# Kernel tuning notes

Measured on AMD Instinct MI355X. Metric: run time of the kernel, lower is better.

## Reference

```python
import jax, jax.numpy as jnp
import numpy as np

N_NODES = 50000
N_EDGES = 312500
WIDTH = 256
LN_EPS = 1e-5


def setup_inputs() -> dict:
    key = jax.random.key(0)
    k1, k2, k3, k4 = jax.random.split(key, 4)
    x = jax.random.normal(k1, (N_NODES, WIDTH), dtype=jnp.float32)
    edge_index = jax.random.randint(k2, (2, N_EDGES), 0, N_NODES, dtype=jnp.int64)
    # GCNConv linear weight (out, in) and bias, LayerNorm affine params
    W = jax.random.normal(k3, (WIDTH, WIDTH), dtype=jnp.float32) / np.sqrt(WIDTH)
    b = jax.random.normal(k4, (WIDTH,), dtype=jnp.float32) * 0.01
    gamma = jnp.ones((WIDTH,), dtype=jnp.float32)
    beta = jnp.zeros((WIDTH,), dtype=jnp.float32)
    return {"x": x, "edge_index": edge_index, "W": W, "b": b, "gamma": gamma, "beta": beta}


def gcn_conv(x, edge_index, W, b):
    """PyG GCNConv: add self-loops, symmetric normalization, scatter-add aggregate."""
    n = x.shape[0]
    loops = jnp.arange(n, dtype=edge_index.dtype)
    src = jnp.concatenate([edge_index[0], loops])  # message source
    dst = jnp.concatenate([edge_index[1], loops])  # message destination
    # degree computed on destination nodes (including self-loops)
    deg = jax.ops.segment_sum(jnp.ones_like(dst, dtype=x.dtype), dst, num_segments=n)
    dinv = jnp.where(deg > 0, jax.lax.rsqrt(deg), 0.0)
    norm = dinv[src] * dinv[dst]  # [E+N]
    h = x @ W.T  # [N, width]
    msgs = norm[:, None] * h[src]  # [E+N, width]
    out = jax.ops.segment_sum(msgs, dst, num_segments=n)
    return out + b


def layer_norm(x, gamma, beta):
    mu = jnp.mean(x, axis=-1, keepdims=True)
    var = jnp.mean(jnp.square(x - mu), axis=-1, keepdims=True)
    return (x - mu) * jax.lax.rsqrt(var + LN_EPS) * gamma + beta


def reference(x, edge_index, W, b, gamma, beta):
    h = gcn_conv(x, edge_index, W, b)
    h = layer_norm(h, gamma, beta)
    h = jax.nn.relu(h)
    # dropout is identity in eval mode
    return h
```

## Files before the change

kernel.cpp:

```cpp
#include <hip/hip_runtime.h>
#include <hip/hip_bf16.h>

#define N_NODES 50000
#define N_EDGES 312500
#define WIDTH   256
#define LN_EPS  1e-5f
#define NB_SCAN 196

typedef __attribute__((ext_vector_type(8))) short bf16x8;
typedef __attribute__((ext_vector_type(4))) float f32x4;

__device__ __forceinline__ float bf_lo(unsigned u) { return __uint_as_float(u << 16); }
__device__ __forceinline__ float bf_hi(unsigned u) { return __uint_as_float(u & 0xffff0000u); }

__global__ void count_dst(const int* __restrict__ dst, int* __restrict__ counts, int e) {
    int i = blockIdx.x * blockDim.x + threadIdx.x;
    if (i < e) atomicAdd(&counts[dst[i]], 1);
}

__global__ __launch_bounds__(256) void scan_pass_a(const int* __restrict__ counts,
                                                   int* __restrict__ block_sums, int n) {
    int t = threadIdx.x;
    int i = blockIdx.x * 256 + t;
    int v = (i < n) ? counts[i] : 0;
    #pragma unroll
    for (int off = 32; off > 0; off >>= 1) v += __shfl_down(v, off, 64);
    __shared__ int ws[4];
    if ((t & 63) == 0) ws[t >> 6] = v;
    __syncthreads();
    if (t == 0) block_sums[blockIdx.x] = ws[0] + ws[1] + ws[2] + ws[3];
}

__global__ __launch_bounds__(256) void scan_pass_b(int* __restrict__ block_sums, int nb) {
    int t = threadIdx.x;
    int lane = t & 63, w = t >> 6;
    int v = (t < nb) ? block_sums[t] : 0;
    int inc = v;
    #pragma unroll
    for (int off = 1; off < 64; off <<= 1) {
        int u = __shfl_up(inc, off, 64);
        if (lane >= off) inc += u;
    }
    __shared__ int wsum[4];
    if (lane == 63) wsum[w] = inc;
    __syncthreads();
    int woff = 0;
    for (int k = 0; k < 4; k++) if (k < w) woff += wsum[k];
    if (t < nb) block_sums[t] = inc - v + woff;
}

__global__ __launch_bounds__(256) void scan_pass_c(int* __restrict__ counts,
                                                   const int* __restrict__ block_sums,
                                                   int* __restrict__ offsets,
                                                   float* __restrict__ dinv, int n) {
    int t = threadIdx.x;
    int i = blockIdx.x * 256 + t;
    int lane = t & 63, w = t >> 6;
    int v = (i < n) ? counts[i] : 0;
    int inc = v;
    #pragma unroll
    for (int off = 1; off < 64; off <<= 1) {
        int u = __shfl_up(inc, off, 64);
        if (lane >= off) inc += u;
    }
    __shared__ int wsum[4];
    if (lane == 63) wsum[w] = inc;
    __syncthreads();
    int woff = 0;
    for (int k = 0; k < 4; k++) if (k < w) woff += wsum[k];
    int excl = block_sums[blockIdx.x] + inc - v + woff;
    if (i < n) {
        offsets[i] = excl;
        counts[i]  = excl;
        dinv[i]    = rsqrtf((float)(v + 1));
    }
    if (i == n - 1) offsets[n] = N_EDGES;
}

__global__ void fill_csr(const int* __restrict__ src, const int* __restrict__ dst,
                         const float* __restrict__ dinv,
                         int* __restrict__ cursor, int2* __restrict__ csr2, int e) {
    int i = blockIdx.x * blockDim.x + threadIdx.x;
    if (i < e) {
        int s = src[i];
        int pos = atomicAdd(&cursor[dst[i]], 1);
        csr2[pos] = make_int2(s, __float_as_int(dinv[s]));
    }
}

__global__ __launch_bounds__(256) void gemm_mfma(const float* __restrict__ x,
                                                 const float* __restrict__ W,
                                                 __hip_bfloat16* __restrict__ h) {
    __shared__ short As[128][72];
    __shared__ short Bs[128][72];
    const int t    = threadIdx.x;
    const int lane = t & 63;
    const int wv   = t >> 6;
    const int wm   = wv & 1;
    const int wn   = wv >> 1;
    const int lrow = lane & 15;
    const int quad = lane >> 4;
    const int mrow0 = blockIdx.x * 128;
    const int ncol0 = blockIdx.y * 128;

    f32x4 acc[4][4];
    #pragma unroll
    for (int i = 0; i < 4; i++)
        #pragma unroll
        for (int j = 0; j < 4; j++)
            #pragma unroll
            for (int r = 0; r < 4; r++) acc[i][j][r] = 0.0f;

    const int sr = t >> 3;
    const int sg = t & 7;

    for (int kc = 0; kc < 4; kc++) {
        int k0 = kc * 64;
        if (kc) __syncthreads();
        #pragma unroll
        for (int p = 0; p < 4; p++) {
            int r  = p * 32 + sr;
            int gr = mrow0 + r;
            union { __hip_bfloat16 hh[8]; bf16x8 v; } ua;
            if (gr < N_NODES) {
                const float* xp = x + (size_t)gr * WIDTH + k0 + sg * 8;
                float4 f0 = *(const float4*)xp;
                float4 f1 = *(const float4*)(xp + 4);
                ua.hh[0] = __float2bfloat16(f0.x); ua.hh[1] = __float2bfloat16(f0.y);
                ua.hh[2] = __float2bfloat16(f0.z); ua.hh[3] = __float2bfloat16(f0.w);
                ua.hh[4] = __float2bfloat16(f1.x); ua.hh[5] = __float2bfloat16(f1.y);
                ua.hh[6] = __float2bfloat16(f1.z); ua.hh[7] = __float2bfloat16(f1.w);
            } else {
                ua.v = (bf16x8){0,0,0,0,0,0,0,0};
            }
            *(bf16x8*)&As[r][sg * 8] = ua.v;

            int gn = ncol0 + r;
            const float* wp = W + (size_t)gn * WIDTH + k0 + sg * 8;
            float4 g0 = *(const float4*)wp;
            float4 g1 = *(const float4*)(wp + 4);
            union { __hip_bfloat16 hh[8]; bf16x8 v; } ub;
            ub.hh[0] = __float2bfloat16(g0.x); ub.hh[1] = __float2bfloat16(g0.y);
            ub.hh[2] = __float2bfloat16(g0.z); ub.hh[3] = __float2bfloat16(g0.w);
            ub.hh[4] = __float2bfloat16(g1.x); ub.hh[5] = __float2bfloat16(g1.y);
            ub.hh[6] = __float2bfloat16(g1.z); ub.hh[7] = __float2bfloat16(g1.w);
            *(bf16x8*)&Bs[r][sg * 8] = ub.v;
        }
        __syncthreads();

        #pragma unroll
        for (int s = 0; s < 2; s++) {
            bf16x8 af[4], bfr[4];
            #pragma unroll
            for (int i = 0; i < 4; i++)
                af[i] = *(const bf16x8*)&As[wm * 64 + i * 16 + lrow][s * 32 + quad * 8];
            #pragma unroll
            for (int j = 0; j < 4; j++)
                bfr[j] = *(const bf16x8*)&Bs[wn * 64 + j * 16 + lrow][s * 32 + quad * 8];
            #pragma unroll
            for (int i = 0; i < 4; i++)
                #pragma unroll
                for (int j = 0; j < 4; j++)
                    acc[i][j] = __builtin_amdgcn_mfma_f32_16x16x32_bf16(
                        af[i], bfr[j], acc[i][j], 0, 0, 0);
        }
    }

    #pragma unroll
    for (int i = 0; i < 4; i++) {
        #pragma unroll
        for (int j = 0; j < 4; j++) {
            int col = ncol0 + wn * 64 + j * 16 + lrow;
            #pragma unroll
            for (int r = 0; r < 4; r++) {
                int gr = mrow0 + wm * 64 + i * 16 + quad * 4 + r;
                if (gr < N_NODES)
                    h[(size_t)gr * WIDTH + col] = __float2bfloat16(acc[i][j][r]);
            }
        }
    }
}

__global__ __launch_bounds__(256) void gather_ln(const __hip_bfloat16* __restrict__ h,
                                                 const float* __restrict__ dinv,
                                                 const int* __restrict__ offsets,
                                                 const int2* __restrict__ csr2,
                                                 const float* __restrict__ b,
                                                 const float* __restrict__ gamma,
                                                 const float* __restrict__ beta,
                                                 float* __restrict__ out) {
    const int lane = threadIdx.x & 63;
    const int d    = blockIdx.x * 4 + (threadIdx.x >> 6);

    const uint2* hrows = (const uint2*)h;
    int beg = offsets[d], end = offsets[d + 1];
    float dv = dinv[d];

    uint2 hv = hrows[(size_t)d * 64 + lane];
    float a0 = dv * bf_lo(hv.x), a1 = dv * bf_hi(hv.x);
    float a2 = dv * bf_lo(hv.y), a3 = dv * bf_hi(hv.y);

    for (int base = beg; base < end; base += 64) {
        int cnt = min(end - base, 64);
        int   s  = 0;
        float sv = 0.0f;
        if (lane < cnt) {
            int2 p = csr2[base + lane];
            s  = p.x;
            sv = __int_as_float(p.y);
        }
        int q = 0;
        for (; q + 4 <= cnt; q += 4) {
            int   s0 = __shfl(s, q, 64),     s1 = __shfl(s, q + 1, 64);
            int   s2 = __shfl(s, q + 2, 64), s3 = __shfl(s, q + 3, 64);
            float w0 = __shfl(sv, q, 64),     w1 = __shfl(sv, q + 1, 64);
            float w2 = __shfl(sv, q + 2, 64), w3 = __shfl(sv, q + 3, 64);
            uint2 r0 = hrows[(size_t)s0 * 64 + lane];
            uint2 r1 = hrows[(size_t)s1 * 64 + lane];
            uint2 r2 = hrows[(size_t)s2 * 64 + lane];
            uint2 r3 = hrows[(size_t)s3 * 64 + lane];
            a0 += w0 * bf_lo(r0.x); a1 += w0 * bf_hi(r0.x);
            a2 += w0 * bf_lo(r0.y); a3 += w0 * bf_hi(r0.y);
            a0 += w1 * bf_lo(r1.x); a1 += w1 * bf_hi(r1.x);
            a2 += w1 * bf_lo(r1.y); a3 += w1 * bf_hi(r1.y);
            a0 += w2 * bf_lo(r2.x); a1 += w2 * bf_hi(r2.x);
            a2 += w2 * bf_lo(r2.y); a3 += w2 * bf_hi(r2.y);
            a0 += w3 * bf_lo(r3.x); a1 += w3 * bf_hi(r3.x);
            a2 += w3 * bf_lo(r3.y); a3 += w3 * bf_hi(r3.y);
        }
        for (; q < cnt; q++) {
            int   sq  = __shfl(s, q, 64);
            float svq = __shfl(sv, q, 64);
            uint2 rv  = hrows[(size_t)sq * 64 + lane];
            a0 += svq * bf_lo(rv.x);
            a1 += svq * bf_hi(rv.x);
            a2 += svq * bf_lo(rv.y);
            a3 += svq * bf_hi(rv.y);
        }
    }

    float4 bv = *(const float4*)(b + lane * 4);
    float v0 = bv.x + dv * a0;
    float v1 = bv.y + dv * a1;
    float v2 = bv.z + dv * a2;
    float v3 = bv.w + dv * a3;

    float s1 = v0 + v1 + v2 + v3;
    float s2 = v0 * v0 + v1 * v1 + v2 * v2 + v3 * v3;
    #pragma unroll
    for (int off = 32; off > 0; off >>= 1) {
        s1 += __shfl_xor(s1, off, 64);
        s2 += __shfl_xor(s2, off, 64);
    }
    float mu   = s1 * (1.0f / 256.0f);
    float var  = s2 * (1.0f / 256.0f) - mu * mu;
    float rstd = rsqrtf(var + LN_EPS);

    float4 gv = *(const float4*)(gamma + lane * 4);
    float4 bt = *(const float4*)(beta + lane * 4);
    float4 y;
    y.x = fmaxf((v0 - mu) * rstd * gv.x + bt.x, 0.0f);
    y.y = fmaxf((v1 - mu) * rstd * gv.y + bt.y, 0.0f);
    y.z = fmaxf((v2 - mu) * rstd * gv.z + bt.z, 0.0f);
    y.w = fmaxf((v3 - mu) * rstd * gv.w + bt.w, 0.0f);
    *(float4*)(out + (size_t)d * WIDTH + lane * 4) = y;
}

extern "C" void kernel_launch(void* const* d_in, const int* in_sizes, int n_in,
                              void* d_out, int out_size, void* d_ws, size_t ws_size,
                              hipStream_t stream) {
    const float* x     = (const float*)d_in[0];
    const int*   ei    = (const int*)d_in[1];
    const float* W     = (const float*)d_in[2];
    const float* b     = (const float*)d_in[3];
    const float* gamma = (const float*)d_in[4];
    const float* beta  = (const float*)d_in[5];
    float* out = (float*)d_out;

    const int* src = ei;
    const int* dst = ei + N_EDGES;

    const int n = N_NODES, e = N_EDGES;

    float* wsf = (float*)d_ws;
    float*          dinv       = wsf;
    __hip_bfloat16* h          = (__hip_bfloat16*)(wsf + 50048);
    int*            counts     = (int*)(wsf + 6450048);
    int*            offsets    = (int*)(wsf + 6500048);
    int*            block_sums = (int*)(wsf + 6550052);
    int2*           csr2       = (int2*)(wsf + 6550310);

    hipMemsetAsync(counts, 0, n * sizeof(int), stream);

    count_dst  <<<(e + 255) / 256, 256, 0, stream>>>(dst, counts, e);
    scan_pass_a<<<NB_SCAN, 256, 0, stream>>>(counts, block_sums, n);
    scan_pass_b<<<1, 256, 0, stream>>>(block_sums, NB_SCAN);
    scan_pass_c<<<NB_SCAN, 256, 0, stream>>>(counts, block_sums, offsets, dinv, n);
    fill_csr   <<<(e + 255) / 256, 256, 0, stream>>>(src, dst, dinv, counts, csr2, e);

    dim3 ggrid((N_NODES + 127) / 128, 2);
    gemm_mfma<<<ggrid, 256, 0, stream>>>(x, W, h);

    gather_ln<<<n / 4, 256, 0, stream>>>(h, dinv, offsets, csr2, b, gamma, beta, out);
}
```

Measured before the change: 205.8 us.

## Load GEMM operands directly from global memory and widen gather unroll to 8

The GEMM drops its shared-memory staging and syncthreads barriers, so each lane loads and converts its own MFMA fragments straight from global memory, clamping out-of-range rows instead of zero-filling. Separately, the neighbour gather loop is unrolled from 4 to 8 rows to keep more independent loads in flight. The GEMM change removes LDS traffic and barriers but makes every wave reload the shared A and B data from global or cache, which adds redundant global loads. Clamped rows only feed outputs that are masked at store time, so correctness holds.

```diff
diff --git a/kernel.cpp b/kernel.cpp
--- a/kernel.cpp
+++ b/kernel.cpp
@@ -12,6 +12,15 @@
 
 __device__ __forceinline__ float bf_lo(unsigned u) { return __uint_as_float(u << 16); }
 __device__ __forceinline__ float bf_hi(unsigned u) { return __uint_as_float(u & 0xffff0000u); }
+
+__device__ __forceinline__ bf16x8 cvt8(float4 a, float4 b) {
+    union { __hip_bfloat16 hh[8]; bf16x8 v; } u;
+    u.hh[0] = __float2bfloat16(a.x); u.hh[1] = __float2bfloat16(a.y);
+    u.hh[2] = __float2bfloat16(a.z); u.hh[3] = __float2bfloat16(a.w);
+    u.hh[4] = __float2bfloat16(b.x); u.hh[5] = __float2bfloat16(b.y);
+    u.hh[6] = __float2bfloat16(b.z); u.hh[7] = __float2bfloat16(b.w);
+    return u.v;
+}
 
 __global__ void count_dst(const int* __restrict__ dst, int* __restrict__ counts, int e) {
     int i = blockIdx.x * blockDim.x + threadIdx.x;
@@ -91,8 +100,6 @@
 __global__ __launch_bounds__(256) void gemm_mfma(const float* __restrict__ x,
                                                  const float* __restrict__ W,
                                                  __hip_bfloat16* __restrict__ h) {
-    __shared__ short As[128][72];
-    __shared__ short Bs[128][72];
     const int t    = threadIdx.x;
     const int lane = t & 63;
     const int wv   = t >> 6;
@@ -103,6 +110,20 @@
     const int mrow0 = blockIdx.x * 128;
     const int ncol0 = blockIdx.y * 128;
 
+    const float* aptr[4];
+    #pragma unroll
+    for (int i = 0; i < 4; i++) {
+        int gr = mrow0 + wm * 64 + i * 16 + lrow;
+        gr = min(gr, N_NODES - 1);
+        aptr[i] = x + (size_t)gr * WIDTH + quad * 8;
+    }
+    const float* bptr[4];
+    #pragma unroll
+    for (int j = 0; j < 4; j++) {
+        int gc = ncol0 + wn * 64 + j * 16 + lrow;
+        bptr[j] = W + (size_t)gc * WIDTH + quad * 8;
+    }
+
     f32x4 acc[4][4];
     #pragma unroll
     for (int i = 0; i < 4; i++)
@@ -111,59 +132,28 @@
             #pragma unroll
             for (int r = 0; r < 4; r++) acc[i][j][r] = 0.0f;
 
-    const int sr = t >> 3;
-    const int sg = t & 7;
-
-    for (int kc = 0; kc < 4; kc++) {
-        int k0 = kc * 64;
-        if (kc) __syncthreads();
-        #pragma unroll
-        for (int p = 0; p < 4; p++) {
-            int r  = p * 32 + sr;
-            int gr = mrow0 + r;
-            union { __hip_bfloat16 hh[8]; bf16x8 v; } ua;
-            if (gr < N_NODES) {
-                const float* xp = x + (size_t)gr * WIDTH + k0 + sg * 8;
-                float4 f0 = *(const float4*)xp;
-                float4 f1 = *(const float4*)(xp + 4);
-                ua.hh[0] = __float2bfloat16(f0.x); ua.hh[1] = __float2bfloat16(f0.y);
-                ua.hh[2] = __float2bfloat16(f0.z); ua.hh[3] = __float2bfloat16(f0.w);
-                ua.hh[4] = __float2bfloat16(f1.x); ua.hh[5] = __float2bfloat16(f1.y);
-                ua.hh[6] = __float2bfloat16(f1.z); ua.hh[7] = __float2bfloat16(f1.w);
-            } else {
-                ua.v = (bf16x8){0,0,0,0,0,0,0,0};
-            }
-            *(bf16x8*)&As[r][sg * 8] = ua.v;
-
-            int gn = ncol0 + r;
-            const float* wp = W + (size_t)gn * WIDTH + k0 + sg * 8;
-            float4 g0 = *(const float4*)wp;
-            float4 g1 = *(const float4*)(wp + 4);
-            union { __hip_bfloat16 hh[8]; bf16x8 v; } ub;
-            ub.hh[0] = __float2bfloat16(g0.x); ub.hh[1] = __float2bfloat16(g0.y);
-            ub.hh[2] = __float2bfloat16(g0.z); ub.hh[3] = __float2bfloat16(g0.w);
-            ub.hh[4] = __float2bfloat16(g1.x); ub.hh[5] = __float2bfloat16(g1.y);
-            ub.hh[6] = __float2bfloat16(g1.z); ub.hh[7] = __float2bfloat16(g1.w);
-            *(bf16x8*)&Bs[r][sg * 8] = ub.v;
-        }
-        __syncthreads();
-
-        #pragma unroll
-        for (int s = 0; s < 2; s++) {
-            bf16x8 af[4], bfr[4];
-            #pragma unroll
-            for (int i = 0; i < 4; i++)
-                af[i] = *(const bf16x8*)&As[wm * 64 + i * 16 + lrow][s * 32 + quad * 8];
+    #pragma unroll 2
+    for (int kc = 0; kc < 8; kc++) {
+        int k0 = kc * 32;
+        bf16x8 af[4], bfr[4];
+        #pragma unroll
+        for (int i = 0; i < 4; i++) {
+            float4 f0 = *(const float4*)(aptr[i] + k0);
+            float4 f1 = *(const float4*)(aptr[i] + k0 + 4);
+            af[i] = cvt8(f0, f1);
+        }
+        #pragma unroll
+        for (int j = 0; j < 4; j++) {
+            float4 g0 = *(const float4*)(bptr[j] + k0);
+            float4 g1 = *(const float4*)(bptr[j] + k0 + 4);
+            bfr[j] = cvt8(g0, g1);
+        }
+        #pragma unroll
+        for (int i = 0; i < 4; i++)
             #pragma unroll
             for (int j = 0; j < 4; j++)
-                bfr[j] = *(const bf16x8*)&Bs[wn * 64 + j * 16 + lrow][s * 32 + quad * 8];
-            #pragma unroll
-            for (int i = 0; i < 4; i++)
-                #pragma unroll
-                for (int j = 0; j < 4; j++)
-                    acc[i][j] = __builtin_amdgcn_mfma_f32_16x16x32_bf16(
-                        af[i], bfr[j], acc[i][j], 0, 0, 0);
-        }
+                acc[i][j] = __builtin_amdgcn_mfma_f32_16x16x32_bf16(
+                    af[i], bfr[j], acc[i][j], 0, 0, 0);
     }
 
     #pragma unroll
@@ -210,23 +200,21 @@
             sv = __int_as_float(p.y);
         }
         int q = 0;
-        for (; q + 4 <= cnt; q += 4) {
-            int   s0 = __shfl(s, q, 64),     s1 = __shfl(s, q + 1, 64);
-            int   s2 = __shfl(s, q + 2, 64), s3 = __shfl(s, q + 3, 64);
-            float w0 = __shfl(sv, q, 64),     w1 = __shfl(sv, q + 1, 64);
-            float w2 = __shfl(sv, q + 2, 64), w3 = __shfl(sv, q + 3, 64);
-            uint2 r0 = hrows[(size_t)s0 * 64 + lane];
-            uint2 r1 = hrows[(size_t)s1 * 64 + lane];
-            uint2 r2 = hrows[(size_t)s2 * 64 + lane];
-            uint2 r3 = hrows[(size_t)s3 * 64 + lane];
-            a0 += w0 * bf_lo(r0.x); a1 += w0 * bf_hi(r0.x);
-            a2 += w0 * bf_lo(r0.y); a3 += w0 * bf_hi(r0.y);
-            a0 += w1 * bf_lo(r1.x); a1 += w1 * bf_hi(r1.x);
-            a2 += w1 * bf_lo(r1.y); a3 += w1 * bf_hi(r1.y);
-            a0 += w2 * bf_lo(r2.x); a1 += w2 * bf_hi(r2.x);
-            a2 += w2 * bf_lo(r2.y); a3 += w2 * bf_hi(r2.y);
-            a0 += w3 * bf_lo(r3.x); a1 += w3 * bf_hi(r3.x);
-            a2 += w3 * bf_lo(r3.y); a3 += w3 * bf_hi(r3.y);
+        for (; q + 8 <= cnt; q += 8) {
+            int   si[8]; float wi[8]; uint2 ri[8];
+            #pragma unroll
+            for (int u = 0; u < 8; u++) {
+                si[u] = __shfl(s, q + u, 64);
+                wi[u] = __shfl(sv, q + u, 64);
+            }
+            #pragma unroll
+            for (int u = 0; u < 8; u++)
+                ri[u] = hrows[(size_t)si[u] * 64 + lane];
+            #pragma unroll
+            for (int u = 0; u < 8; u++) {
+                a0 += wi[u] * bf_lo(ri[u].x); a1 += wi[u] * bf_hi(ri[u].x);
+                a2 += wi[u] * bf_lo(ri[u].y); a3 += wi[u] * bf_hi(ri[u].y);
+            }
         }
         for (; q < cnt; q++) {
             int   sq  = __shfl(s, q, 64);
```

Result: slower. 230.6 us (+12.1%).
